# Kernel tuning notes

Measured on AMD Instinct MI355X. Metric: run time of the kernel, lower is better.

## Reference

```python
import jax, jax.numpy as jnp
import numpy as np

N_NODES = 50000
N_EDGES = 1600000
HEADS = 4
EMB = 16          # per-head output features
HIDDEN = 256
BATCH = 1024
IN_FEAT = 4       # num_node_features (hard-coded in source)
NEG_SLOPE = 0.2   # PyG GATConv default leaky_relu slope


def setup_inputs() -> dict:
    key = jax.random.key(0)
    ks = jax.random.split(key, 8)
    out_dim = HEADS * EMB
    return {
        "message": jax.random.normal(ks[0], (BATCH, HIDDEN), dtype=jnp.float32),
        "x": jax.random.normal(ks[1], (N_NODES, IN_FEAT), dtype=jnp.float32),
        "edge_index": jax.random.randint(ks[2], (2, N_EDGES), 0, N_NODES, dtype=jnp.int64)
                      if jax.config.read("jax_enable_x64") else
                      jax.random.randint(ks[2], (2, N_EDGES), 0, N_NODES, dtype=jnp.int32),
        "gat_w": jax.random.normal(ks[3], (IN_FEAT, out_dim), dtype=jnp.float32) * 0.5,
        "att_src": jax.random.normal(ks[4], (HEADS, EMB), dtype=jnp.float32) * 0.25,
        "att_dst": jax.random.normal(ks[5], (HEADS, EMB), dtype=jnp.float32) * 0.25,
        "gat_b": jnp.zeros((out_dim,), dtype=jnp.float32),
        "fc_w": jax.random.normal(ks[6], (HIDDEN, out_dim), dtype=jnp.float32) * (1.0 / np.sqrt(HIDDEN)),
        "fc_b": jnp.zeros((out_dim,), dtype=jnp.float32),
    }


def reference(message, x, edge_index, gat_w, att_src, att_dst, gat_b, fc_w, fc_b):
    N = x.shape[0]
    H, F = att_src.shape
    src, dst = edge_index[0], edge_index[1]

    # --- GATConv (single layer, concat heads) ---
    h = (x @ gat_w).reshape(N, H, F)                       # [N,H,F]
    a_s = jnp.einsum('nhf,hf->nh', h, att_src)             # per-node src score
    a_d = jnp.einsum('nhf,hf->nh', h, att_dst)             # per-node dst score
    e = jax.nn.leaky_relu(a_s[src] + a_d[dst], NEG_SLOPE)  # [E,H]

    # stable softmax over edges grouped by destination node
    m = jax.ops.segment_max(e, dst, num_segments=N)        # [N,H]
    ex = jnp.exp(e - m[dst])                               # [E,H]
    denom = jax.ops.segment_sum(ex, dst, num_segments=N)   # [N,H]
    alpha = ex / (denom[dst] + 1e-16)                      # [E,H]

    # weighted aggregation of source features into destinations
    agg = jax.ops.segment_sum(alpha[:, :, None] * h[src], dst, num_segments=N)  # [N,H,F]
    h_out = agg.reshape(N, H * F) + gat_b                  # [N, H*F]

    # --- fc + matmul + log_softmax ---
    msg_emb = message @ fc_w + fc_b                        # [B, H*F]
    logits = (h_out @ msg_emb.T).T                         # [B, N]
    return jax.nn.log_softmax(logits, axis=1)
```

## Files before the change

### kernel.cpp

```cpp
#include <hip/hip_runtime.h>
#include <math.h>

#define N_NODES 50000
#define N_EDGES 1600000
#define HEADS 4
#define EMB 16
#define HOUT 64
#define HIDDEN 256
#define BATCH 1024
#define NEG_SLOPE 0.2f
#define ATS 50176
#define SCAN_NB 196
#define NXCD 8
#define DRANGE 6250
#define NSTRIP 196
#define NT32 1563

typedef __attribute__((ext_vector_type(8))) short bf16x8;
typedef __attribute__((ext_vector_type(16))) float f32x16;

__device__ __forceinline__ float lrelu(float x) { return x > 0.f ? x : NEG_SLOPE * x; }

__device__ __forceinline__ ushort f2bf(float f) {
    unsigned u = __float_as_uint(f);
    return (ushort)((u + 0x7fffu + ((u >> 16) & 1u)) >> 16);
}
__device__ __forceinline__ float bf2f(ushort h) { return __uint_as_float(((unsigned)h) << 16); }

__global__ void k_msgemb(const float* __restrict__ msg, const float* __restrict__ fcw,
                         const float* __restrict__ fcb,
                         ushort* __restrict__ msg_hi, ushort* __restrict__ msg_lo) {
    __shared__ float mrow[HIDDEN];
    int b = blockIdx.x;
    int j = threadIdx.x;
    for (int k = j; k < HIDDEN; k += 64) mrow[k] = msg[b * HIDDEN + k];
    __syncthreads();
    float acc = fcb[j];
    #pragma unroll 8
    for (int k = 0; k < HIDDEN; k++) acc += mrow[k] * fcw[k * HOUT + j];
    ushort hi = f2bf(acc);
    msg_hi[b * HOUT + j] = hi;
    msg_lo[b * HOUT + j] = f2bf(acc - bf2f(hi));
}

__global__ void k_node(const float* __restrict__ x, const float* __restrict__ gatw,
                       const float* __restrict__ atts, const float* __restrict__ attd,
                       float* __restrict__ h, float* __restrict__ a_s, float* __restrict__ a_d) {
    int tid = blockIdx.x * blockDim.x + threadIdx.x;
    int n = tid >> 6;
    int j = tid & 63;
    if (n >= N_NODES) return;
    float4 xv = ((const float4*)x)[n];
    float hv = xv.x * gatw[j] + xv.y * gatw[64 + j] + xv.z * gatw[128 + j] + xv.w * gatw[192 + j];
    h[n * 64 + j] = hv;
    float s = hv * atts[j];
    float d = hv * attd[j];
    for (int o = 8; o > 0; o >>= 1) {
        s += __shfl_down(s, o, 16);
        d += __shfl_down(d, o, 16);
    }
    if ((j & 15) == 0) {
        int head = j >> 4;
        a_s[n * 4 + head] = s;
        a_d[n * 4 + head] = d;
    }
}

__global__ void k_count(const int* __restrict__ ei, int* __restrict__ cnt) {
    int p = blockIdx.x & 7;
    int tile = blockIdx.x >> 3;
    int e = tile * 256 + threadIdx.x;
    if (e < N_EDGES) {
        int d = ei[N_EDGES + e];
        if ((unsigned)(d - p * DRANGE) < (unsigned)DRANGE)
            atomicAdd(&cnt[d], 1);
    }
}

__global__ void k_scan1(const int* __restrict__ cnt, int* __restrict__ localx,
                        int* __restrict__ partial) {
    int b = blockIdx.x, t = threadIdx.x;
    int i = b * 256 + t;
    int v = (i < N_NODES) ? cnt[i] : 0;
    int lane = t & 63, w = t >> 6;
    int sv = v;
    #pragma unroll
    for (int o = 1; o < 64; o <<= 1) {
        int u = __shfl_up(sv, o);
        if (lane >= o) sv += u;
    }
    __shared__ int wsums[4];
    if (lane == 63) wsums[w] = sv;
    __syncthreads();
    int woff = 0;
    #pragma unroll
    for (int k = 0; k < 4; k++) woff += (k < w) ? wsums[k] : 0;
    if (i < N_NODES) localx[i] = woff + sv - v;
    if (t == 0) partial[b] = wsums[0] + wsums[1] + wsums[2] + wsums[3];
}

__global__ void k_scan2(const int* __restrict__ partial, int* __restrict__ blockoff,
                        int* __restrict__ rowptr_last) {
    int t = threadIdx.x;
    int v = (t < SCAN_NB) ? partial[t] : 0;
    int lane = t & 63, w = t >> 6;
    int sv = v;
    #pragma unroll
    for (int o = 1; o < 64; o <<= 1) {
        int u = __shfl_up(sv, o);
        if (lane >= o) sv += u;
    }
    __shared__ int wsums[4];
    if (lane == 63) wsums[w] = sv;
    __syncthreads();
    int woff = 0;
    #pragma unroll
    for (int k = 0; k < 4; k++) woff += (k < w) ? wsums[k] : 0;
    int excl = woff + sv - v;
    if (t < SCAN_NB) blockoff[t] = excl;
    if (t == 255) rowptr_last[0] = excl + v;
}

__global__ void k_scan3(const int* __restrict__ localx, const int* __restrict__ blockoff,
                        int* __restrict__ rowptr, int* __restrict__ cursor) {
    int i = blockIdx.x * 256 + threadIdx.x;
    if (i < N_NODES) {
        int r = localx[i] + blockoff[blockIdx.x];
        rowptr[i] = r;
        cursor[i] = r;
    }
}

__global__ void k_scatter(const int* __restrict__ ei, int* __restrict__ cursor, int* __restrict__ csr) {
    int p = blockIdx.x & 7;
    int tile = blockIdx.x >> 3;
    int e = tile * 256 + threadIdx.x;
    if (e < N_EDGES) {
        int d = ei[N_EDGES + e];
        if ((unsigned)(d - p * DRANGE) < (unsigned)DRANGE) {
            int pos = atomicAdd(&cursor[d], 1);
            csr[pos] = ei[e];
        }
    }
}

__global__ __launch_bounds__(256, 8) void k_agg(const int* __restrict__ rowptr,
                      const int* __restrict__ csr,
                      const float* __restrict__ a_s, const float* __restrict__ a_d,
                      const float* __restrict__ h,
                      ushort* __restrict__ agg_hi, ushort* __restrict__ agg_lo) {
    __shared__ float salpha[4][64];
    int wid = threadIdx.x >> 6;
    int lane = threadIdx.x & 63;
    int n = blockIdx.x * 4 + wid;
    if (n >= N_NODES) return;
    int beg = rowptr[n], end = rowptr[n + 1];
    int head = lane & 3, eoff = lane >> 2;
    float adh = a_d[n * 4 + head];

    float s = 0.f;
    for (int i = beg + eoff; i < end; i += 16) {
        int src = csr[i];
        s += __expf(lrelu(a_s[src * 4 + head] + adh));
    }
    #pragma unroll
    for (int o = 4; o < 64; o <<= 1) s += __shfl_xor(s, o);
    float inv = 1.f / (s + 1e-16f);

    float acc = 0.f;
    const float* ap = &salpha[wid][(lane >> 4) * 16];
    for (int base = beg; base < end; base += 16) {
        int e = base + eoff;
        int ec = (e < end) ? e : (end - 1);
        int src = csr[ec];
        float ev = lrelu(a_s[src * 4 + head] + adh);
        float alpha = (e < end) ? __expf(ev) * inv : 0.f;
        salpha[wid][head * 16 + eoff] = alpha;
        __builtin_amdgcn_wave_barrier();
        #pragma unroll
        for (int c = 0; c < 4; c++) {
            float4 av = *(const float4*)(ap + c * 4);
            int s0 = __builtin_amdgcn_readlane(src, c * 16 + 0);
            int s1 = __builtin_amdgcn_readlane(src, c * 16 + 4);
            int s2 = __builtin_amdgcn_readlane(src, c * 16 + 8);
            int s3 = __builtin_amdgcn_readlane(src, c * 16 + 12);
            acc = fmaf(av.x, h[(size_t)s0 * 64 + lane], acc);
            acc = fmaf(av.y, h[(size_t)s1 * 64 + lane], acc);
            acc = fmaf(av.z, h[(size_t)s2 * 64 + lane], acc);
            acc = fmaf(av.w, h[(size_t)s3 * 64 + lane], acc);
        }
        __builtin_amdgcn_wave_barrier();
    }
    ushort hi = f2bf(acc);
    agg_hi[(size_t)n * 64 + lane] = hi;
    agg_lo[(size_t)n * 64 + lane] = f2bf(acc - bf2f(hi));
}


__global__ __launch_bounds__(256, 4) void k_logsum(const ushort* __restrict__ agg_hi,
    const ushort* __restrict__ agg_lo, const ushort* __restrict__ msg_hi,
    const ushort* __restrict__ msg_lo, float* __restrict__ ps) {
    int t = threadIdx.x;
    int lane = t & 63, wid = t >> 6;
    int l31 = lane & 31, half = lane >> 5;
    int b0 = blockIdx.y * 32;
    int gw = blockIdx.x * 4 + wid;

    const ushort* mh = msg_hi + (size_t)(b0 + l31) * HOUT + half * 8;
    const ushort* ml = msg_lo + (size_t)(b0 + l31) * HOUT + half * 8;
    bf16x8 mH[4], mL[4];
    #pragma unroll
    for (int ks = 0; ks < 4; ks++) {
        mH[ks] = *(const bf16x8*)(mh + ks * 16);
        mL[ks] = *(const bf16x8*)(ml + ks * 16);
    }

    float sacc[16];
    #pragma unroll
    for (int r = 0; r < 16; r++) sacc[r] = 0.f;

    for (int i = 0; i < 8; i++) {
        int tile = gw * 8 + i;
        int n0 = tile * 32;
        if (n0 >= N_NODES) break;
        const ushort* ah = agg_hi + (size_t)(n0 + l31) * HOUT + half * 8;
        const ushort* al = agg_lo + (size_t)(n0 + l31) * HOUT + half * 8;
        f32x16 acc;
        #pragma unroll
        for (int r = 0; r < 16; r++) acc[r] = 0.f;
        #pragma unroll
        for (int ks = 0; ks < 4; ks++) {
            bf16x8 aH = *(const bf16x8*)(ah + ks * 16);
            bf16x8 aL = *(const bf16x8*)(al + ks * 16);
            acc = __builtin_amdgcn_mfma_f32_32x32x16_bf16(mH[ks], aH, acc, 0, 0, 0);
            acc = __builtin_amdgcn_mfma_f32_32x32x16_bf16(mH[ks], aL, acc, 0, 0, 0);
            acc = __builtin_amdgcn_mfma_f32_32x32x16_bf16(mL[ks], aH, acc, 0, 0, 0);
        }
        bool valid = (n0 + l31) < N_NODES;
        #pragma unroll
        for (int r = 0; r < 16; r++) sacc[r] += valid ? __expf(acc[r]) : 0.f;
    }
    #pragma unroll
    for (int r = 0; r < 16; r++) {
        float s = sacc[r];
        #pragma unroll
        for (int o = 1; o < 32; o <<= 1) s += __shfl_xor(s, o);
        sacc[r] = s;
    }
    if (l31 == 0) {
        #pragma unroll
        for (int r = 0; r < 16; r++) {
            int b = b0 + (r & 3) + 8 * (r >> 2) + 4 * half;
            ps[(size_t)b * NSTRIP + gw] = sacc[r];
        }
    }
}

__global__ void k_rowstats(const float* __restrict__ ps, float* __restrict__ rowls) {
    int b = blockIdx.x * blockDim.x + threadIdx.x;
    if (b >= BATCH) return;
    float S = 0.f;
    for (int i = 0; i < NSTRIP; i++) S += ps[b * NSTRIP + i];
    rowls[b] = logf(S);
}

__global__ __launch_bounds__(256, 4) void k_logits_w(const ushort* __restrict__ agg_hi,
    const ushort* __restrict__ agg_lo, const ushort* __restrict__ msg_hi,
    const ushort* __restrict__ msg_lo, const float* __restrict__ rowls,
    float* __restrict__ out) {
    int t = threadIdx.x;
    int lane = t & 63, wid = t >> 6;
    int l31 = lane & 31, half = lane >> 5;
    int b0 = blockIdx.y * 32;
    int gw = blockIdx.x * 4 + wid;

    const ushort* mh = msg_hi + (size_t)(b0 + l31) * HOUT + half * 8;
    const ushort* ml = msg_lo + (size_t)(b0 + l31) * HOUT + half * 8;
    bf16x8 mH[4], mL[4];
    #pragma unroll
    for (int ks = 0; ks < 4; ks++) {
        mH[ks] = *(const bf16x8*)(mh + ks * 16);
        mL[ks] = *(const bf16x8*)(ml + ks * 16);
    }
    float sub[16];
    int brow[16];
    #pragma unroll
    for (int r = 0; r < 16; r++) {
        brow[r] = b0 + (r & 3) + 8 * (r >> 2) + 4 * half;
        sub[r] = rowls[brow[r]];
    }

    for (int i = 0; i < 8; i++) {
        int tile = gw * 8 + i;
        int n0 = tile * 32;
        if (n0 >= N_NODES) break;
        const ushort* ah = agg_hi + (size_t)(n0 + l31) * HOUT + half * 8;
        const ushort* al = agg_lo + (size_t)(n0 + l31) * HOUT + half * 8;
        f32x16 acc;
        #pragma unroll
        for (int r = 0; r < 16; r++) acc[r] = 0.f;
        #pragma unroll
        for (int ks = 0; ks < 4; ks++) {
            bf16x8 aH = *(const bf16x8*)(ah + ks * 16);
            bf16x8 aL = *(const bf16x8*)(al + ks * 16);
            acc = __builtin_amdgcn_mfma_f32_32x32x16_bf16(mH[ks], aH, acc, 0, 0, 0);
            acc = __builtin_amdgcn_mfma_f32_32x32x16_bf16(mH[ks], aL, acc, 0, 0, 0);
            acc = __builtin_amdgcn_mfma_f32_32x32x16_bf16(mL[ks], aH, acc, 0, 0, 0);
        }
        int n = n0 + l31;
        if (n < N_NODES) {
            #pragma unroll
            for (int r = 0; r < 16; r++)
                out[(size_t)brow[r] * N_NODES + n] = acc[r] - sub[r];
        }
    }
}

extern "C" void kernel_launch(void* const* d_in, const int* in_sizes, int n_in,
                              void* d_out, int out_size, void* d_ws, size_t ws_size,
                              hipStream_t stream) {
    const float* message = (const float*)d_in[0];
    const float* x       = (const float*)d_in[1];
    const int*   ei      = (const int*)d_in[2];
    const float* gat_w   = (const float*)d_in[3];
    const float* att_src = (const float*)d_in[4];
    const float* att_dst = (const float*)d_in[5];
    const float* fc_w    = (const float*)d_in[7];
    const float* fc_b    = (const float*)d_in[8];
    float* out = (float*)d_out;

    float* ws      = (float*)d_ws;
    float* a_s     = ws;
    float* a_d     = a_s + (size_t)N_NODES * HEADS;
    float* hbuf    = a_d + (size_t)N_NODES * HEADS;
    float* ps      = hbuf + (size_t)N_NODES * HOUT;
    float* rowls   = ps + (size_t)BATCH * NSTRIP;
    ushort* msg_hi = (ushort*)(rowls + BATCH);
    ushort* msg_lo = msg_hi + (size_t)BATCH * HOUT;
    ushort* agg_hi = msg_lo + (size_t)BATCH * HOUT;
    ushort* agg_lo = agg_hi + (size_t)ATS * HOUT;
    int*   cnt     = (int*)(agg_lo + (size_t)ATS * HOUT);
    int*   rowptr  = cnt + N_NODES;
    int*   cursor  = rowptr + N_NODES + 1;
    int*   csr     = cursor + N_NODES;
    int*   localx  = csr + N_EDGES;
    int*   partial = localx + N_NODES;
    int*   blockoff= partial + SCAN_NB;

    hipMemsetAsync(cnt, 0, N_NODES * sizeof(int), stream);
    k_msgemb<<<BATCH, 64, 0, stream>>>(message, fc_w, fc_b, msg_hi, msg_lo);
    k_node<<<(N_NODES * 64 + 255) / 256, 256, 0, stream>>>(x, gat_w, att_src, att_dst, hbuf, a_s, a_d);
    k_count<<<NXCD * (N_EDGES / 256), 256, 0, stream>>>(ei, cnt);
    k_scan1<<<SCAN_NB, 256, 0, stream>>>(cnt, localx, partial);
    k_scan2<<<1, 256, 0, stream>>>(partial, blockoff, rowptr + N_NODES);
    k_scan3<<<SCAN_NB, 256, 0, stream>>>(localx, blockoff, rowptr, cursor);
    k_scatter<<<NXCD * (N_EDGES / 256), 256, 0, stream>>>(ei, cursor, csr);
    k_agg<<<(N_NODES + 3) / 4, 256, 0, stream>>>(rowptr, csr, a_s, a_d, hbuf, agg_hi, agg_lo);
    dim3 g4(49, 32);
    k_logsum<<<g4, 256, 0, stream>>>(agg_hi, agg_lo, msg_hi, msg_lo, ps);
    k_rowstats<<<4, 256, 0, stream>>>(ps, rowls);
    k_logits_w<<<g4, 256, 0, stream>>>(agg_hi, agg_lo, msg_hi, msg_lo, rowls, out);
}
```

Before: 608.6 us.

## Swap loop order in logsum and logits kernels to keep node tiles in registers

Both GEMM-style kernels now hold a node tile's agg_hi/agg_lo fragments in registers and loop over batch groups, streaming the small msg embedding, where before they held msg and streamed agg. Logsum reduces per-batch exp sums into a shared-memory array with atomics and writes one partial row per block. Logits processes two node tiles per wave against 256 batch rows per block, caching row log-sums in shared memory. The goal is to cut repeated agg reads from global memory and raise MFMA work per load, at the cost of more registers (launch bounds lowered to 3) and shared atomics.

```diff
diff --git a/kernel.cpp b/kernel.cpp
--- a/kernel.cpp
+++ b/kernel.cpp
@@ -13,8 +13,8 @@
 #define SCAN_NB 196
 #define NXCD 8
 #define DRANGE 6250
-#define NSTRIP 196
-#define NT32 1563
+#define NLBLK 392
+#define NPBLK 196
 
 typedef __attribute__((ext_vector_type(8))) short bf16x8;
 typedef __attribute__((ext_vector_type(16))) float f32x16;
@@ -200,59 +200,52 @@
 __global__ __launch_bounds__(256, 4) void k_logsum(const ushort* __restrict__ agg_hi,
     const ushort* __restrict__ agg_lo, const ushort* __restrict__ msg_hi,
     const ushort* __restrict__ msg_lo, float* __restrict__ ps) {
+    __shared__ float bsum[BATCH];
     int t = threadIdx.x;
+    #pragma unroll
+    for (int i = 0; i < 4; i++) bsum[i * 256 + t] = 0.f;
+    __syncthreads();
     int lane = t & 63, wid = t >> 6;
     int l31 = lane & 31, half = lane >> 5;
-    int b0 = blockIdx.y * 32;
-    int gw = blockIdx.x * 4 + wid;
-
-    const ushort* mh = msg_hi + (size_t)(b0 + l31) * HOUT + half * 8;
-    const ushort* ml = msg_lo + (size_t)(b0 + l31) * HOUT + half * 8;
-    bf16x8 mH[4], mL[4];
+    int tile = blockIdx.x * 4 + wid;
+    int n0 = tile * 32;
+    bool vcol = (n0 + l31) < N_NODES;
+    const ushort* ah = agg_hi + (size_t)(n0 + l31) * HOUT + half * 8;
+    const ushort* al = agg_lo + (size_t)(n0 + l31) * HOUT + half * 8;
+    bf16x8 aH[4], aL[4];
     #pragma unroll
     for (int ks = 0; ks < 4; ks++) {
-        mH[ks] = *(const bf16x8*)(mh + ks * 16);
-        mL[ks] = *(const bf16x8*)(ml + ks * 16);
-    }
-
-    float sacc[16];
-    #pragma unroll
-    for (int r = 0; r < 16; r++) sacc[r] = 0.f;
-
-    for (int i = 0; i < 8; i++) {
-        int tile = gw * 8 + i;
-        int n0 = tile * 32;
-        if (n0 >= N_NODES) break;
-        const ushort* ah = agg_hi + (size_t)(n0 + l31) * HOUT + half * 8;
-        const ushort* al = agg_lo + (size_t)(n0 + l31) * HOUT + half * 8;
+        aH[ks] = *(const bf16x8*)(ah + ks * 16);
+        aL[ks] = *(const bf16x8*)(al + ks * 16);
+    }
+    for (int g = 0; g < 32; g++) {
+        const ushort* mh = msg_hi + (size_t)(g * 32 + l31) * HOUT + half * 8;
+        const ushort* ml = msg_lo + (size_t)(g * 32 + l31) * HOUT + half * 8;
         f32x16 acc;
         #pragma unroll
         for (int r = 0; r < 16; r++) acc[r] = 0.f;
         #pragma unroll
         for (int ks = 0; ks < 4; ks++) {
-            bf16x8 aH = *(const bf16x8*)(ah + ks * 16);
-            bf16x8 aL = *(const bf16x8*)(al + ks * 16);
-            acc = __builtin_amdgcn_mfma_f32_32x32x16_bf16(mH[ks], aH, acc, 0, 0, 0);
-            acc = __builtin_amdgcn_mfma_f32_32x32x16_bf16(mH[ks], aL, acc, 0, 0, 0);
-            acc = __builtin_amdgcn_mfma_f32_32x32x16_bf16(mL[ks], aH, acc, 0, 0, 0);
-        }
-        bool valid = (n0 + l31) < N_NODES;
-        #pragma unroll
-        for (int r = 0; r < 16; r++) sacc[r] += valid ? __expf(acc[r]) : 0.f;
-    }
-    #pragma unroll
-    for (int r = 0; r < 16; r++) {
-        float s = sacc[r];
-        #pragma unroll
-        for (int o = 1; o < 32; o <<= 1) s += __shfl_xor(s, o);
-        sacc[r] = s;
-    }
-    if (l31 == 0) {
+            bf16x8 mH = *(const bf16x8*)(mh + ks * 16);
+            bf16x8 mL = *(const bf16x8*)(ml + ks * 16);
+            acc = __builtin_amdgcn_mfma_f32_32x32x16_bf16(mH, aH[ks], acc, 0, 0, 0);
+            acc = __builtin_amdgcn_mfma_f32_32x32x16_bf16(mH, aL[ks], acc, 0, 0, 0);
+            acc = __builtin_amdgcn_mfma_f32_32x32x16_bf16(mL, aH[ks], acc, 0, 0, 0);
+        }
         #pragma unroll
         for (int r = 0; r < 16; r++) {
-            int b = b0 + (r & 3) + 8 * (r >> 2) + 4 * half;
-            ps[(size_t)b * NSTRIP + gw] = sacc[r];
-        }
+            float s = vcol ? __expf(acc[r]) : 0.f;
+            #pragma unroll
+            for (int o = 1; o < 32; o <<= 1) s += __shfl_xor(s, o);
+            if (l31 == 0)
+                atomicAdd(&bsum[g * 32 + (r & 3) + 8 * (r >> 2) + 4 * half], s);
+        }
+    }
+    __syncthreads();
+    #pragma unroll
+    for (int i = 0; i < 4; i++) {
+        int b = i * 256 + t;
+        ps[(size_t)blockIdx.x * BATCH + b] = bsum[b];
     }
 }
 
@@ -260,58 +253,60 @@
     int b = blockIdx.x * blockDim.x + threadIdx.x;
     if (b >= BATCH) return;
     float S = 0.f;
-    for (int i = 0; i < NSTRIP; i++) S += ps[b * NSTRIP + i];
+    for (int i = 0; i < NLBLK; i++) S += ps[(size_t)i * BATCH + b];
     rowls[b] = logf(S);
 }
 
-__global__ __launch_bounds__(256, 4) void k_logits_w(const ushort* __restrict__ agg_hi,
+__global__ __launch_bounds__(256, 3) void k_logits_w(const ushort* __restrict__ agg_hi,
     const ushort* __restrict__ agg_lo, const ushort* __restrict__ msg_hi,
     const ushort* __restrict__ msg_lo, const float* __restrict__ rowls,
     float* __restrict__ out) {
+    __shared__ float subs[256];
     int t = threadIdx.x;
+    int bbase = blockIdx.y * 256;
+    subs[t] = rowls[bbase + t];
+    __syncthreads();
     int lane = t & 63, wid = t >> 6;
     int l31 = lane & 31, half = lane >> 5;
-    int b0 = blockIdx.y * 32;
-    int gw = blockIdx.x * 4 + wid;
-
-    const ushort* mh = msg_hi + (size_t)(b0 + l31) * HOUT + half * 8;
-    const ushort* ml = msg_lo + (size_t)(b0 + l31) * HOUT + half * 8;
-    bf16x8 mH[4], mL[4];
+    int tp = blockIdx.x * 4 + wid;
+    int n0 = tp * 64, n1 = n0 + 32;
+    bool v0 = (n0 + l31) < N_NODES, v1 = (n1 + l31) < N_NODES;
+    const ushort* ah0 = agg_hi + (size_t)(n0 + l31) * HOUT + half * 8;
+    const ushort* al0 = agg_lo + (size_t)(n0 + l31) * HOUT + half * 8;
+    const ushort* ah1 = agg_hi + (size_t)(n1 + l31) * HOUT + half * 8;
+    const ushort* al1 = agg_lo + (size_t)(n1 + l31) * HOUT + half * 8;
+    bf16x8 aH0[4], aL0[4], aH1[4], aL1[4];
     #pragma unroll
     for (int ks = 0; ks < 4; ks++) {
-        mH[ks] = *(const bf16x8*)(mh + ks * 16);
-        mL[ks] = *(const bf16x8*)(ml + ks * 16);
-    }
-    float sub[16];
-    int brow[16];
-    #pragma unroll
-    for (int r = 0; r < 16; r++) {
-        brow[r] = b0 + (r & 3) + 8 * (r >> 2) + 4 * half;
-        sub[r] = rowls[brow[r]];
-    }
-
-    for (int i = 0; i < 8; i++) {
-        int tile = gw * 8 + i;
-        int n0 = tile * 32;
-        if (n0 >= N_NODES) break;
-        const ushort* ah = agg_hi + (size_t)(n0 + l31) * HOUT + half * 8;
-        const ushort* al = agg_lo + (size_t)(n0 + l31) * HOUT + half * 8;
-        f32x16 acc;
-        #pragma unroll
-        for (int r = 0; r < 16; r++) acc[r] = 0.f;
+        aH0[ks] = *(const bf16x8*)(ah0 + ks * 16);
+        aL0[ks] = *(const bf16x8*)(al0 + ks * 16);
+        aH1[ks] = *(const bf16x8*)(ah1 + ks * 16);
+        aL1[ks] = *(const bf16x8*)(al1 + ks * 16);
+    }
+    for (int g = 0; g < 8; g++) {
+        const ushort* mh = msg_hi + (size_t)(bbase + g * 32 + l31) * HOUT + half * 8;
+        const ushort* ml = msg_lo + (size_t)(bbase + g * 32 + l31) * HOUT + half * 8;
+        f32x16 acc0, acc1;
+        #pragma unroll
+        for (int r = 0; r < 16; r++) { acc0[r] = 0.f; acc1[r] = 0.f; }
         #pragma unroll
         for (int ks = 0; ks < 4; ks++) {
-            bf16x8 aH = *(const bf16x8*)(ah + ks * 16);
-            bf16x8 aL = *(const bf16x8*)(al + ks * 16);
-            acc = __builtin_amdgcn_mfma_f32_32x32x16_bf16(mH[ks], aH, acc, 0, 0, 0);
-            acc = __builtin_amdgcn_mfma_f32_32x32x16_bf16(mH[ks], aL, acc, 0, 0, 0);
-            acc = __builtin_amdgcn_mfma_f32_32x32x16_bf16(mL[ks], aH, acc, 0, 0, 0);
-        }
-        int n = n0 + l31;
-        if (n < N_NODES) {
-            #pragma unroll
-            for (int r = 0; r < 16; r++)
-                out[(size_t)brow[r] * N_NODES + n] = acc[r] - sub[r];
+            bf16x8 mH = *(const bf16x8*)(mh + ks * 16);
+            bf16x8 mL = *(const bf16x8*)(ml + ks * 16);
+            acc0 = __builtin_amdgcn_mfma_f32_32x32x16_bf16(mH, aH0[ks], acc0, 0, 0, 0);
+            acc0 = __builtin_amdgcn_mfma_f32_32x32x16_bf16(mH, aL0[ks], acc0, 0, 0, 0);
+            acc0 = __builtin_amdgcn_mfma_f32_32x32x16_bf16(mL, aH0[ks], acc0, 0, 0, 0);
+            acc1 = __builtin_amdgcn_mfma_f32_32x32x16_bf16(mH, aH1[ks], acc1, 0, 0, 0);
+            acc1 = __builtin_amdgcn_mfma_f32_32x32x16_bf16(mH, aL1[ks], acc1, 0, 0, 0);
+            acc1 = __builtin_amdgcn_mfma_f32_32x32x16_bf16(mL, aH1[ks], acc1, 0, 0, 0);
+        }
+        #pragma unroll
+        for (int r = 0; r < 16; r++) {
+            int lr = g * 32 + (r & 3) + 8 * (r >> 2) + 4 * half;
+            float sub = subs[lr];
+            size_t rowoff = (size_t)(bbase + lr) * N_NODES;
+            if (v0) out[rowoff + n0 + l31] = acc0[r] - sub;
+            if (v1) out[rowoff + n1 + l31] = acc1[r] - sub;
         }
     }
 }
@@ -334,7 +329,7 @@
     float* a_d     = a_s + (size_t)N_NODES * HEADS;
     float* hbuf    = a_d + (size_t)N_NODES * HEADS;
     float* ps      = hbuf + (size_t)N_NODES * HOUT;
-    float* rowls   = ps + (size_t)BATCH * NSTRIP;
+    float* rowls   = ps + (size_t)NLBLK * BATCH;
     ushort* msg_hi = (ushort*)(rowls + BATCH);
     ushort* msg_lo = msg_hi + (size_t)BATCH * HOUT;
     ushort* agg_hi = msg_lo + (size_t)BATCH * HOUT;
@@ -356,8 +351,8 @@
     k_scan3<<<SCAN_NB, 256, 0, stream>>>(localx, blockoff, rowptr, cursor);
     k_scatter<<<NXCD * (N_EDGES / 256), 256, 0, stream>>>(ei, cursor, csr);
     k_agg<<<(N_NODES + 3) / 4, 256, 0, stream>>>(rowptr, csr, a_s, a_d, hbuf, agg_hi, agg_lo);
-    dim3 g4(49, 32);
-    k_logsum<<<g4, 256, 0, stream>>>(agg_hi, agg_lo, msg_hi, msg_lo, ps);
+    k_logsum<<<NLBLK, 256, 0, stream>>>(agg_hi, agg_lo, msg_hi, msg_lo, ps);
     k_rowstats<<<4, 256, 0, stream>>>(ps, rowls);
-    k_logits_w<<<g4, 256, 0, stream>>>(agg_hi, agg_lo, msg_hi, msg_lo, rowls, out);
-}
+    dim3 gw(NPBLK, 4);
+    k_logits_w<<<gw, 256, 0, stream>>>(agg_hi, agg_lo, msg_hi, msg_lo, rowls, out);
+}
```

Measured after the change: 621.2 us. 2.1% more time.
